# Performance work log

Measured on AMD Instinct MI355X. Metric: run time of the kernel, lower is better.

Reference implementation:

```python
import jax, jax.numpy as jnp
import numpy as np

D_MODEL = 1024
NUM_HEADS = 16
D_K = D_MODEL // NUM_HEADS
SCALE = 1.0 / np.sqrt(D_K).astype(np.float32)


def _rope_cos_sin(T, d_k):
    inv_freq = 1.0 / (10000.0 ** (jnp.arange(0, d_k, 2, dtype=jnp.float32) / d_k))
    t = jnp.arange(T, dtype=jnp.float32)
    freqs = jnp.outer(t, inv_freq)                      # [T, d_k/2]
    emb = jnp.concatenate([freqs, freqs], axis=-1)      # [T, d_k]
    return jnp.cos(emb)[None, None], jnp.sin(emb)[None, None]  # [1,1,T,d_k]


def _rotate_half(x):
    x1, x2 = x[..., : x.shape[-1] // 2], x[..., x.shape[-1] // 2 :]
    return jnp.concatenate([-x2, x1], axis=-1)


def setup_inputs() -> dict:
    key = jax.random.key(0)
    ks = jax.random.split(key, 8)
    B, T, C = 2, 2048, D_MODEL
    x = jax.random.normal(ks[0], (B, T, C), dtype=jnp.float32)
    # torch nn.Linear weights are [out, in]; forward does x @ W.T
    s = 1.0 / np.sqrt(C)
    Wq = jax.random.uniform(ks[1], (C, C), jnp.float32, -s, s)
    Wk = jax.random.uniform(ks[2], (C, C), jnp.float32, -s, s)
    Wv = jax.random.uniform(ks[3], (C, C), jnp.float32, -s, s)
    Wo = jax.random.uniform(ks[4], (C, C), jnp.float32, -s, s)
    bo = jax.random.uniform(ks[5], (C,), jnp.float32, -s, s)
    sector_bias = jnp.zeros((1, NUM_HEADS, 1, 1), dtype=jnp.float32)
    sector_weights = jax.random.uniform(ks[6], (B, T), jnp.float32, 0.5, 1.5)
    # causal mask, broadcastable to [B,H,T,T]; 0 -> masked
    mask = jnp.tril(jnp.ones((T, T), dtype=jnp.int32))[None, None]
    return {
        "x": x, "Wq": Wq, "Wk": Wk, "Wv": Wv, "Wo": Wo, "bo": bo,
        "sector_bias": sector_bias, "sector_weights": sector_weights,
        "mask": mask,
    }


def reference(x, Wq, Wk, Wv, Wo, bo, sector_bias, sector_weights, mask):
    B, T, C = x.shape
    H, dk = NUM_HEADS, D_K
    q = (x @ Wq.T).reshape(B, T, H, dk).transpose(0, 2, 1, 3)  # [B,H,T,dk]
    k = (x @ Wk.T).reshape(B, T, H, dk).transpose(0, 2, 1, 3)
    v = (x @ Wv.T).reshape(B, T, H, dk).transpose(0, 2, 1, 3)
    cos, sin = _rope_cos_sin(T, dk)
    q = q * cos + _rotate_half(q) * sin
    k = k * cos + _rotate_half(k) * sin
    scores = jnp.einsum("bhqd,bhkd->bhqk", q, k) * SCALE
    scores = scores + sector_bias
    scores = scores * sector_weights[:, None, None, :]  # broadcast over key dim
    scores = jnp.where(mask == 0, -jnp.inf, scores)
    attn = jax.nn.softmax(scores, axis=-1)
    out = jnp.einsum("bhqk,bhkd->bhqd", attn, v)
    out = out.transpose(0, 2, 1, 3).reshape(B, T, C)
    return out @ Wo.T + bo
```

## Files before the change

kernel.cpp:

```cpp
#include <hip/hip_runtime.h>


typedef __bf16 bf16x8 __attribute__((ext_vector_type(8)));
typedef float f32x4 __attribute__((ext_vector_type(4)));
typedef float f32x16 __attribute__((ext_vector_type(16)));
typedef unsigned short u16x8 __attribute__((ext_vector_type(8)));

__device__ __forceinline__ unsigned short f2bf(float f) {
    union { float f; unsigned int u; } c; c.f = f;
    unsigned int u = c.u;
    unsigned int r = u + 0x7fffu + ((u >> 16) & 1u);
    return (unsigned short)(r >> 16);
}
__device__ __forceinline__ unsigned cvtpk(float lo, float hi) {
    unsigned r;
    asm("v_cvt_pk_bf16_f32 %0, %1, %2" : "=v"(r) : "v"(lo), "v"(hi));
    return r;
}
__device__ __forceinline__ void plswap(unsigned a, unsigned b, unsigned& r0, unsigned& r1) {
#if __has_builtin(__builtin_amdgcn_permlane32_swap)
    auto s = __builtin_amdgcn_permlane32_swap(a, b, false, false);
    r0 = (unsigned)s[0]; r1 = (unsigned)s[1];
#else
    const int hh = (int)(threadIdx.x & 63) >> 5;
    const unsigned oa = (unsigned)__shfl_xor((int)a, 32);
    const unsigned ob = (unsigned)__shfl_xor((int)b, 32);
    r0 = hh ? ob : a;
    r1 = hh ? b : oa;
#endif
}
__device__ __forceinline__ void stage8_f32(unsigned short* dst, const float* src) {
    const float4 a = *(const float4*)src;
    const float4 b = *(const float4*)(src + 4);
    u16x8 v;
    v[0] = f2bf(a.x); v[1] = f2bf(a.y); v[2] = f2bf(a.z); v[3] = f2bf(a.w);
    v[4] = f2bf(b.x); v[5] = f2bf(b.y); v[6] = f2bf(b.z); v[7] = f2bf(b.w);
    *(u16x8*)dst = v;
}
__device__ __forceinline__ void async16(const unsigned short* g, unsigned short* l) {
    __builtin_amdgcn_global_load_lds(
        (const __attribute__((address_space(1))) void*)g,
        (__attribute__((address_space(3))) void*)l, 16, 0, 0);
}

__global__ __launch_bounds__(256) void cvt_all(
    const float* __restrict__ x, const float* __restrict__ Wq, const float* __restrict__ Wk,
    const float* __restrict__ Wv, const float* __restrict__ Wo,
    unsigned short* __restrict__ dst, int hasX, int n8)
{
    const int i = blockIdx.x * 256 + threadIdx.x;
    if (i >= n8) return;
    int r = i;
    const float* src; int off;
    const int xg = hasX ? 524288 : 0;
    if (r < xg) { src = x; off = r; }
    else {
        r -= xg;
        const int w = r >> 17, o = r & 131071;
        src = (w == 0) ? Wq : (w == 1) ? Wk : (w == 2) ? Wv : Wo;
        off = o;
    }
    stage8_f32(&dst[(size_t)i * 8], &src[(size_t)off * 8]);
}

template<int A_BF16>
__global__ __launch_bounds__(256) void gemm_qkv(
    const void* __restrict__ Av, const unsigned short* __restrict__ Wb,
    unsigned short* __restrict__ outv, const float* __restrict__ swg)
{
    constexpr int K = 1024, BK = 32;
    __shared__ __align__(16) unsigned short As[2][128 * BK];
    __shared__ __align__(16) unsigned short Bs[2][128 * BK];
    const int tid = threadIdx.x;
    const int wid = tid >> 6, lane = tid & 63, g = lane >> 4, l = lane & 15;
    const int wm = (wid & 1) * 64, wn = (wid >> 1) * 64;

    const int lin = blockIdx.x + (blockIdx.y << 3) + (blockIdx.z << 8);
    const int wg  = (lin & 7) * 96 + (lin >> 3);
    const int bx = wg & 7, by = (wg >> 3) & 31, bz = wg >> 8;
    const int m0 = by * 128, n0 = bx * 128;
    const int z = bz;
    const unsigned short* W = Wb + (size_t)z * 1048576;

    f32x4 acc[4][4];
#pragma unroll
    for (int i = 0; i < 4; ++i)
#pragma unroll
        for (int j = 0; j < 4; ++j) acc[i][j] = f32x4{0.f, 0.f, 0.f, 0.f};

    const int r = tid >> 2;
    const int c = (tid & 3) * 8;

    auto stage = [&](int buf, int k0) {
        if (A_BF16) {
            const unsigned short* A = (const unsigned short*)Av;
            unsigned short* AsW = &As[buf][wid * 512];
            async16(&A[(size_t)(m0 + r) * K + k0 + c], AsW);
            async16(&A[(size_t)(m0 + 64 + r) * K + k0 + c], AsW + 2048);
        } else {
            const float* A = (const float*)Av;
            stage8_f32(&As[buf][tid * 8],        &A[(size_t)(m0 + r) * K + k0 + c]);
            stage8_f32(&As[buf][tid * 8 + 2048], &A[(size_t)(m0 + 64 + r) * K + k0 + c]);
        }
        unsigned short* BsW = &Bs[buf][wid * 512];
        async16(&W[(size_t)(n0 + r) * K + k0 + c], BsW);
        async16(&W[(size_t)(n0 + 64 + r) * K + k0 + c], BsW + 2048);
    };

    stage(0, 0);
    __syncthreads();

    for (int k0 = 0; k0 < K; k0 += BK) {
        const int cur = (k0 >> 5) & 1;
        if (k0 + BK < K) stage(cur ^ 1, k0 + BK);

        const unsigned short* Asr = As[cur];
        const unsigned short* Bsr = Bs[cur];
        bf16x8 af[4], bfr[4];
#pragma unroll
        for (int im = 0; im < 4; ++im) af[im]  = *(const bf16x8*)&Asr[(wm + im * 16 + l) * BK + g * 8];
#pragma unroll
        for (int in = 0; in < 4; ++in) bfr[in] = *(const bf16x8*)&Bsr[(wn + in * 16 + l) * BK + g * 8];
#pragma unroll
        for (int im = 0; im < 4; ++im)
#pragma unroll
            for (int in = 0; in < 4; ++in)
                acc[im][in] = __builtin_amdgcn_mfma_f32_16x16x32_bf16(af[im], bfr[in], acc[im][in], 0, 0, 0);
        __syncthreads();
    }

    unsigned short* outq = outv + (size_t)z * 4194304;
    if (z < 2) {
        const int hq = (n0 + wn) >> 6;
        float freq[2];
#pragma unroll
        for (int in = 0; in < 2; ++in)
            freq[in] = exp2f(-(float)(in * 16 + l) * 0.41524101186f);
#pragma unroll
        for (int im = 0; im < 4; ++im)
#pragma unroll
            for (int i = 0; i < 4; ++i) {
                const int m = m0 + wm + im * 16 + g * 4 + i;
                const int b = m >> 11, t = m & 2047;
                float fw = 1.0f;
                if (z == 1) fw = 0.18033688011f * swg[(b << 11) + t];
                const size_t fq = (size_t)((b << 4) + hq) * 131072
                                + (size_t)((t >> 5) << 2) * 512
                                + (size_t)((((l >> 3) & 1) << 5) + (t & 31)) * 8 + (l & 7);
#pragma unroll
                for (int in = 0; in < 2; ++in) {
                    const float ang = (float)t * freq[in];
                    const float cs = __cosf(ang), sn = __sinf(ang);
                    const float x1 = acc[im][in][i], x2 = acc[im][in + 2][i];
                    outq[fq + (size_t)in * 512]       = f2bf((x1 * cs - x2 * sn) * fw);
                    outq[fq + (size_t)(in + 2) * 512] = f2bf((x2 * cs + x1 * sn) * fw);
                }
            }
    } else {
#pragma unroll
        for (int im = 0; im < 4; ++im)
#pragma unroll
            for (int in = 0; in < 4; ++in) {
                const int n = n0 + wn + in * 16 + l;
                const int h = n >> 6, d = n & 63;
                const int mb = m0 + wm + im * 16 + g * 4;
                const int bq = mb >> 11, t0 = mb & 2047;
                ushort4 pk;
                pk.x = f2bf(acc[im][in][0]); pk.y = f2bf(acc[im][in][1]);
                pk.z = f2bf(acc[im][in][2]); pk.w = f2bf(acc[im][in][3]);
                const size_t fv = (size_t)((bq << 4) + h) * 131072
                                + (size_t)(((t0 >> 5) << 2) + ((d >> 5) << 1) + ((t0 >> 4) & 1)) * 512
                                + (size_t)((((t0 >> 3) & 1) << 5) + (d & 31)) * 8 + (t0 & 7);
                *(ushort4*)&outq[fv] = pk;
            }
    }
}

__global__ __launch_bounds__(256) void gemm_proj(
    const unsigned short* __restrict__ A, const unsigned short* __restrict__ W,
    float* __restrict__ out, const float* __restrict__ bias)
{
    constexpr int K = 1024, BK = 32;
    __shared__ __align__(16) unsigned short As[2][64 * BK];
    __shared__ __align__(16) unsigned short Bs[2][128 * BK];
    const int tid = threadIdx.x;
    const int wid = tid >> 6, lane = tid & 63, g = lane >> 4, l = lane & 15;
    const int wm = (wid & 1) * 32, wn = (wid >> 1) * 64;

    const int lin = blockIdx.x + (blockIdx.y << 3);
    const int wg  = (lin & 7) * 64 + (lin >> 3);
    const int m0 = (wg >> 3) * 64, n0 = (wg & 7) * 128;

    f32x4 acc[2][4];
#pragma unroll
    for (int i = 0; i < 2; ++i)
#pragma unroll
        for (int j = 0; j < 4; ++j) acc[i][j] = f32x4{0.f, 0.f, 0.f, 0.f};

    const int r = tid >> 2;
    const int c = (tid & 3) * 8;

    auto stage = [&](int buf, int k0) {
        unsigned short* AsW = &As[buf][wid * 512];
        unsigned short* BsW = &Bs[buf][wid * 512];
        async16(&A[(size_t)(m0 + r) * K + k0 + c], AsW);
        async16(&W[(size_t)(n0 + r) * K + k0 + c], BsW);
        async16(&W[(size_t)(n0 + 64 + r) * K + k0 + c], BsW + 2048);
    };

    stage(0, 0);
    __syncthreads();

    for (int k0 = 0; k0 < K; k0 += BK) {
        const int cur = (k0 >> 5) & 1;
        if (k0 + BK < K) stage(cur ^ 1, k0 + BK);

        const unsigned short* Asr = As[cur];
        const unsigned short* Bsr = Bs[cur];
        bf16x8 af[2], bfr[4];
#pragma unroll
        for (int im = 0; im < 2; ++im) af[im]  = *(const bf16x8*)&Asr[(wm + im * 16 + l) * BK + g * 8];
#pragma unroll
        for (int in = 0; in < 4; ++in) bfr[in] = *(const bf16x8*)&Bsr[(wn + in * 16 + l) * BK + g * 8];
#pragma unroll
        for (int im = 0; im < 2; ++im)
#pragma unroll
            for (int in = 0; in < 4; ++in)
                acc[im][in] = __builtin_amdgcn_mfma_f32_16x16x32_bf16(af[im], bfr[in], acc[im][in], 0, 0, 0);
        __syncthreads();
    }

#pragma unroll
    for (int im = 0; im < 2; ++im)
#pragma unroll
        for (int in = 0; in < 4; ++in) {
            const int n = n0 + wn + in * 16 + l;
#pragma unroll
            for (int i = 0; i < 4; ++i) {
                const int m = m0 + wm + im * 16 + g * 4 + i;
                out[(size_t)m * 1024 + n] = acc[im][in][i] + bias[n];
            }
        }
}

__global__ __launch_bounds__(128, 2) void flash_attn(
    const unsigned short* __restrict__ Qf, const unsigned short* __restrict__ Kf,
    const unsigned short* __restrict__ Vf, const float* __restrict__ sbias,
    const float* __restrict__ sw, unsigned short* __restrict__ attn)
{
    constexpr int T = 2048;
    __shared__ float Cmb[3072];

    const int tid = threadIdx.x, wid = tid >> 6, lane = tid & 63;
    const int hl = lane & 31, hh = lane >> 5;
    const int id = blockIdx.x;
    const int p  = 63 - (id >> 5);
    const int bh = id & 31, b = bh >> 4, h = bh & 15;
    const size_t fb = (size_t)bh * 131072;
    const float bias = sbias[h];
    const float* swb = sw + b * T;

    bf16x8 onef;
#pragma unroll
    for (int j = 0; j < 8; ++j) onef[j] = (__bf16)1.0f;

    const int q0 = p * 32;
    bf16x8 qf[4];
#pragma unroll
    for (int ks = 0; ks < 4; ++ks)
        qf[ks] = *(const bf16x8*)&Qf[fb + (size_t)(p * 4 + ks) * 512 + lane * 8];

    f32x16 oacc[2], lrow;
#pragma unroll
    for (int r = 0; r < 16; ++r) { oacc[0][r] = 0.f; oacc[1][r] = 0.f; lrow[r] = 0.f; }

    for (int c = wid; c <= p; c += 2) {
        const unsigned short* kb = &Kf[fb + (size_t)c * 2048 + lane * 8];
        const unsigned short* vb = &Vf[fb + (size_t)c * 2048 + lane * 8];

        const bf16x8 kf0 = *(const bf16x8*)&kb[0];
        const bf16x8 kf1 = *(const bf16x8*)&kb[512];
        const bf16x8 kf2 = *(const bf16x8*)&kb[1024];
        const bf16x8 kf3 = *(const bf16x8*)&kb[1536];
        f32x16 sx;
#pragma unroll
        for (int r = 0; r < 16; ++r) sx[r] = 0.f;
        sx = __builtin_amdgcn_mfma_f32_32x32x16_bf16(kf0, qf[0], sx, 0, 0, 0);
        sx = __builtin_amdgcn_mfma_f32_32x32x16_bf16(kf1, qf[1], sx, 0, 0, 0);
        sx = __builtin_amdgcn_mfma_f32_32x32x16_bf16(kf2, qf[2], sx, 0, 0, 0);
        sx = __builtin_amdgcn_mfma_f32_32x32x16_bf16(kf3, qf[3], sx, 0, 0, 0);

        const bf16x8 vf00 = *(const bf16x8*)&vb[0];
        const bf16x8 vf01 = *(const bf16x8*)&vb[512];
        const bf16x8 vf10 = *(const bf16x8*)&vb[1024];
        const bf16x8 vf11 = *(const bf16x8*)&vb[1536];

        if (bias != 0.0f) {
            const float bn = bias * 1.44269504f;
#pragma unroll
            for (int r = 0; r < 16; ++r) {
                const int kl = (r & 3) + 8 * (r >> 2) + 4 * hh;
                sx[r] += bn * swb[c * 32 + kl];
            }
        }
        if (c == p) {
#pragma unroll
            for (int r = 0; r < 16; ++r) {
                const int kl = (r & 3) + 8 * (r >> 2) + 4 * hh;
                sx[r] = (kl <= hl) ? sx[r] : -1e30f;
            }
        }
#pragma unroll
        for (int r = 0; r < 16; ++r) sx[r] = exp2f(sx[r]);

        unsigned wds[8];
#pragma unroll
        for (int g2 = 0; g2 < 4; ++g2) {
            wds[g2 * 2]     = cvtpk(sx[g2 * 4],     sx[g2 * 4 + 1]);
            wds[g2 * 2 + 1] = cvtpk(sx[g2 * 4 + 2], sx[g2 * 4 + 3]);
        }
        bf16x8 pf[2];
#pragma unroll
        for (int ks = 0; ks < 2; ++ks) {
            unsigned a0, a1, b0, b1;
            plswap(wds[4 * ks],     wds[4 * ks + 2], a0, a1);
            plswap(wds[4 * ks + 1], wds[4 * ks + 3], b0, b1);
            union { unsigned u[4]; bf16x8 v; } pk_;
            pk_.u[0] = a0; pk_.u[1] = b0;
            pk_.u[2] = a1; pk_.u[3] = b1;
            pf[ks] = pk_.v;
        }

        lrow = __builtin_amdgcn_mfma_f32_32x32x16_bf16(pf[0], onef, lrow, 0, 0, 0);
        lrow = __builtin_amdgcn_mfma_f32_32x32x16_bf16(pf[1], onef, lrow, 0, 0, 0);

        oacc[0] = __builtin_amdgcn_mfma_f32_32x32x16_bf16(pf[0], vf00, oacc[0], 0, 0, 0);
        oacc[0] = __builtin_amdgcn_mfma_f32_32x32x16_bf16(pf[1], vf01, oacc[0], 0, 0, 0);
        oacc[1] = __builtin_amdgcn_mfma_f32_32x32x16_bf16(pf[0], vf10, oacc[1], 0, 0, 0);
        oacc[1] = __builtin_amdgcn_mfma_f32_32x32x16_bf16(pf[1], vf11, oacc[1], 0, 0, 0);
    }

    __syncthreads();
    if (wid == 1) {
#pragma unroll
        for (int dt = 0; dt < 2; ++dt)
#pragma unroll
            for (int r = 0; r < 16; ++r) Cmb[(dt * 16 + r) * 64 + lane] = oacc[dt][r];
#pragma unroll
        for (int r = 0; r < 16; ++r) Cmb[2048 + r * 64 + lane] = lrow[r];
    }
    __syncthreads();
    if (wid == 0) {
#pragma unroll
        for (int r = 0; r < 16; ++r) {
            const float li = 1.0f / (lrow[r] + Cmb[2048 + r * 64 + lane]);
            const int row = (r & 3) + 8 * (r >> 2) + 4 * hh;
            const int qr = q0 + row;
#pragma unroll
            for (int dt = 0; dt < 2; ++dt) {
                const float ov = oacc[dt][r] + Cmb[(dt * 16 + r) * 64 + lane];
                attn[(size_t)(b * T + qr) * 1024 + h * 64 + dt * 32 + hl] = f2bf(ov * li);
            }
        }
    }
}

extern "C" void kernel_launch(void* const* d_in, const int* in_sizes, int n_in,
                              void* d_out, int out_size, void* d_ws, size_t ws_size,
                              hipStream_t stream) {
    const float* x  = (const float*)d_in[0];
    const float* Wq = (const float*)d_in[1];
    const float* Wk = (const float*)d_in[2];
    const float* Wv = (const float*)d_in[3];
    const float* Wo = (const float*)d_in[4];
    const float* bo = (const float*)d_in[5];
    const float* sb = (const float*)d_in[6];
    const float* sw = (const float*)d_in[7];

    const size_t QKV_SZ = 4194304;
    const size_t W_SZ   = 1048576;
    unsigned short* ws16 = (unsigned short*)d_ws;
    const bool big = ws_size >= 2 * (4 * QKV_SZ + 4 * W_SZ);

    if (big) {
        unsigned short* xb    = ws16;
        unsigned short* Wb3   = xb + QKV_SZ;
        unsigned short* Wob   = Wb3 + 3 * W_SZ;
        unsigned short* qkv   = Wob + W_SZ;
        unsigned short* attnb = xb;

        cvt_all<<<4096, 256, 0, stream>>>(x, Wq, Wk, Wv, Wo, xb, 1, 1048576);
        gemm_qkv<1><<<dim3(8, 32, 3), 256, 0, stream>>>(xb, Wb3, qkv, sw);
        flash_attn<<<2048, 128, 0, stream>>>(qkv, qkv + QKV_SZ, qkv + 2 * QKV_SZ,
                                             sb, sw, attnb);
        gemm_proj<<<dim3(8, 64), 256, 0, stream>>>(attnb, Wob, (float*)d_out, bo);
    } else {
        unsigned short* qkv   = ws16;
        unsigned short* attnb = qkv + 3 * QKV_SZ;
        unsigned short* Wb3   = attnb;
        unsigned short* Wob   = qkv;

        cvt_all<<<1536, 256, 0, stream>>>(x, Wq, Wk, Wv, Wo, Wb3, 0, 393216);
        gemm_qkv<0><<<dim3(8, 32, 3), 256, 0, stream>>>(x, Wb3, qkv, sw);
        flash_attn<<<2048, 128, 0, stream>>>(qkv, qkv + QKV_SZ, qkv + 2 * QKV_SZ,
                                             sb, sw, attnb);
        cvt_all<<<512, 256, 0, stream>>>(x, Wo, Wo, Wo, Wo, Wob, 0, 131072);
        gemm_proj<<<dim3(8, 64), 256, 0, stream>>>(attnb, Wob, (float*)d_out, bo);
    }
}
```

Before: 194.5 us.

## Triple-buffer GEMM K-loop with explicit vmcnt waits and single barrier

Converts the bf16-input QKV GEMM and the output projection GEMM from double-buffered LDS staging with two syncthreads per step to a three-stage ring. Each step waits on a partial vmcnt and issues one s_barrier, so two tiles of async loads stay in flight while the MFMAs run. This hides global-load latency and removes one barrier per K step, at the cost of 50% more LDS per block, which may lower occupancy. Correctness depends on the hardcoded vmcnt counts matching the number of async loads issued per stage.

```diff
diff --git a/kernel.cpp b/kernel.cpp
--- a/kernel.cpp
+++ b/kernel.cpp
@@ -68,9 +68,9 @@
     const void* __restrict__ Av, const unsigned short* __restrict__ Wb,
     unsigned short* __restrict__ outv, const float* __restrict__ swg)
 {
-    constexpr int K = 1024, BK = 32;
-    __shared__ __align__(16) unsigned short As[2][128 * BK];
-    __shared__ __align__(16) unsigned short Bs[2][128 * BK];
+    constexpr int K = 1024, BK = 32, NS = K / BK;
+    __shared__ __align__(16) unsigned short As[3][128 * BK];
+    __shared__ __align__(16) unsigned short Bs[3][128 * BK];
     const int tid = threadIdx.x;
     const int wid = tid >> 6, lane = tid & 63, g = lane >> 4, l = lane & 15;
     const int wm = (wid & 1) * 64, wn = (wid >> 1) * 64;
@@ -92,30 +92,17 @@
     const int c = (tid & 3) * 8;
 
     auto stage = [&](int buf, int k0) {
-        if (A_BF16) {
-            const unsigned short* A = (const unsigned short*)Av;
-            unsigned short* AsW = &As[buf][wid * 512];
-            async16(&A[(size_t)(m0 + r) * K + k0 + c], AsW);
-            async16(&A[(size_t)(m0 + 64 + r) * K + k0 + c], AsW + 2048);
-        } else {
-            const float* A = (const float*)Av;
-            stage8_f32(&As[buf][tid * 8],        &A[(size_t)(m0 + r) * K + k0 + c]);
-            stage8_f32(&As[buf][tid * 8 + 2048], &A[(size_t)(m0 + 64 + r) * K + k0 + c]);
-        }
+        const unsigned short* A = (const unsigned short*)Av;
+        unsigned short* AsW = &As[buf][wid * 512];
+        async16(&A[(size_t)(m0 + r) * K + k0 + c], AsW);
+        async16(&A[(size_t)(m0 + 64 + r) * K + k0 + c], AsW + 2048);
         unsigned short* BsW = &Bs[buf][wid * 512];
         async16(&W[(size_t)(n0 + r) * K + k0 + c], BsW);
         async16(&W[(size_t)(n0 + 64 + r) * K + k0 + c], BsW + 2048);
     };
-
-    stage(0, 0);
-    __syncthreads();
-
-    for (int k0 = 0; k0 < K; k0 += BK) {
-        const int cur = (k0 >> 5) & 1;
-        if (k0 + BK < K) stage(cur ^ 1, k0 + BK);
-
-        const unsigned short* Asr = As[cur];
-        const unsigned short* Bsr = Bs[cur];
+    auto compute = [&](int buf) {
+        const unsigned short* Asr = As[buf];
+        const unsigned short* Bsr = Bs[buf];
         bf16x8 af[4], bfr[4];
 #pragma unroll
         for (int im = 0; im < 4; ++im) af[im]  = *(const bf16x8*)&Asr[(wm + im * 16 + l) * BK + g * 8];
@@ -126,7 +113,35 @@
 #pragma unroll
             for (int in = 0; in < 4; ++in)
                 acc[im][in] = __builtin_amdgcn_mfma_f32_16x16x32_bf16(af[im], bfr[in], acc[im][in], 0, 0, 0);
+    };
+
+    if (A_BF16) {
+        stage(0, 0);
+        stage(1, BK);
+        for (int ks = 0; ks < NS; ++ks) {
+            if (ks + 1 < NS) asm volatile("s_waitcnt vmcnt(4)" ::: "memory");
+            else             asm volatile("s_waitcnt vmcnt(0)" ::: "memory");
+            __builtin_amdgcn_s_barrier();
+            compute(ks % 3);
+            if (ks + 2 < NS) stage((ks + 2) % 3, (ks + 2) * BK);
+        }
+    } else {
+        auto stageF = [&](int buf, int k0) {
+            const float* A = (const float*)Av;
+            stage8_f32(&As[buf][tid * 8],        &A[(size_t)(m0 + r) * K + k0 + c]);
+            stage8_f32(&As[buf][tid * 8 + 2048], &A[(size_t)(m0 + 64 + r) * K + k0 + c]);
+            unsigned short* BsW = &Bs[buf][wid * 512];
+            async16(&W[(size_t)(n0 + r) * K + k0 + c], BsW);
+            async16(&W[(size_t)(n0 + 64 + r) * K + k0 + c], BsW + 2048);
+        };
+        stageF(0, 0);
         __syncthreads();
+        for (int k0 = 0; k0 < K; k0 += BK) {
+            const int cur = (k0 >> 5) & 1;
+            if (k0 + BK < K) stageF(cur ^ 1, k0 + BK);
+            compute(cur);
+            __syncthreads();
+        }
     }
 
     unsigned short* outq = outv + (size_t)z * 4194304;
@@ -180,9 +195,9 @@
     const unsigned short* __restrict__ A, const unsigned short* __restrict__ W,
     float* __restrict__ out, const float* __restrict__ bias)
 {
-    constexpr int K = 1024, BK = 32;
-    __shared__ __align__(16) unsigned short As[2][64 * BK];
-    __shared__ __align__(16) unsigned short Bs[2][128 * BK];
+    constexpr int K = 1024, BK = 32, NS = K / BK;
+    __shared__ __align__(16) unsigned short As[3][64 * BK];
+    __shared__ __align__(16) unsigned short Bs[3][128 * BK];
     const int tid = threadIdx.x;
     const int wid = tid >> 6, lane = tid & 63, g = lane >> 4, l = lane & 15;
     const int wm = (wid & 1) * 32, wn = (wid >> 1) * 64;
@@ -209,14 +224,13 @@
     };
 
     stage(0, 0);
-    __syncthreads();
-
-    for (int k0 = 0; k0 < K; k0 += BK) {
-        const int cur = (k0 >> 5) & 1;
-        if (k0 + BK < K) stage(cur ^ 1, k0 + BK);
-
-        const unsigned short* Asr = As[cur];
-        const unsigned short* Bsr = Bs[cur];
+    stage(1, BK);
+    for (int ks = 0; ks < NS; ++ks) {
+        if (ks + 1 < NS) asm volatile("s_waitcnt vmcnt(3)" ::: "memory");
+        else             asm volatile("s_waitcnt vmcnt(0)" ::: "memory");
+        __builtin_amdgcn_s_barrier();
+        const unsigned short* Asr = As[ks % 3];
+        const unsigned short* Bsr = Bs[ks % 3];
         bf16x8 af[2], bfr[4];
 #pragma unroll
         for (int im = 0; im < 2; ++im) af[im]  = *(const bf16x8*)&Asr[(wm + im * 16 + l) * BK + g * 8];
@@ -227,7 +241,7 @@
 #pragma unroll
             for (int in = 0; in < 4; ++in)
                 acc[im][in] = __builtin_amdgcn_mfma_f32_16x16x32_bf16(af[im], bfr[in], acc[im][in], 0, 0, 0);
-        __syncthreads();
+        if (ks + 2 < NS) stage((ks + 2) % 3, (ks + 2) * BK);
     }
 
 #pragma unroll
```

Result: faster. 188.2 us (-3.2%).
